# Kernel optimization log

Measured on AMD Instinct MI355X. Metric: run time of the kernel, lower is better.

## Reference

```python
import jax, jax.numpy as jnp
import numpy as np

N_R = 256          # number of relations
N_HOP_MAX = 3      # max hops
N_E = 200_000      # number of entities
N_T = 1_000_000    # number of KB triples
B = 32             # batch size
D_Q = 768          # BERT question embedding dim
D_IN = D_Q + (N_HOP_MAX - 1) * N_R  # input width of dense_inf / dense_att


def setup_inputs() -> dict:
    key = jax.random.key(0)
    ks = jax.random.split(key, 7)
    x = (jax.random.uniform(ks[0], (B, N_E)) < 0.001).astype(jnp.float32)
    h_q = jax.random.normal(ks[1], (B, D_Q), jnp.float32)
    W_inf = jax.random.normal(ks[2], (N_R, D_IN), jnp.float32) * 0.02
    W_att = jax.random.normal(ks[3], (1, D_IN), jnp.float32) * 0.02
    subj_idx = jax.random.randint(ks[4], (N_T,), 0, N_E, jnp.int32)
    rel_idx = jax.random.randint(ks[5], (N_T,), 0, N_R, jnp.int32)
    obj_idx = jax.random.randint(ks[6], (N_T,), 0, N_E, jnp.int32)
    return {"x": x, "h_q": h_q, "W_inf": W_inf, "W_att": W_att,
            "subj_idx": subj_idx, "rel_idx": rel_idx, "obj_idx": obj_idx,
            "n_hop": N_HOP_MAX}


def _one_step(x, r, subj_idx, rel_idx, obj_idx):
    # Equivalent to ((x @ M_subj.T) * (r @ M_rel.T)) @ M_obj with 0/1
    # indicator matrices: gather - elementwise multiply - scatter-add.
    x_t = jnp.take(x, subj_idx, axis=1)   # (B, N_T)
    r_t = jnp.take(r, rel_idx, axis=1)    # (B, N_T)
    prod = x_t * r_t                       # (B, N_T)
    # scatter-add over triples into object entities: (N_T, B) -> (N_E, B)
    return jax.ops.segment_sum(prod.T, obj_idx, num_segments=x.shape[1]).T


def reference(x, h_q, W_inf, W_att, subj_idx, rel_idx, obj_idx, n_hop):
    rs, cs, xs = [], [], []
    for i in range(n_hop):
        if i:
            # most-recent relation first, then older ones (rs[::-1])
            concat = jnp.concatenate([h_q] + rs[::-1], axis=1)
        else:
            concat = h_q
        pad = jnp.zeros((h_q.shape[0], (N_HOP_MAX - 1 - i) * N_R), h_q.dtype)
        concat = jnp.concatenate([concat, pad], axis=1)  # (B, D_IN)
        r = concat @ W_inf.T   # (B, N_R)
        c = concat @ W_att.T   # (B, 1)
        x = _one_step(x, r, subj_idx, rel_idx, obj_idx)  # (B, N_E)
        rs.append(r)
        cs.append(c)
        xs.append(x)
    a = jax.nn.softmax(jnp.concatenate(cs, axis=1), axis=-1)  # (B, n_hop)
    y = jnp.einsum('bh,bhe->be', a, jnp.stack(xs, axis=1))     # (B, N_E)
    return y
```

## Files before the change

kernel.cpp:

```cpp
#include <hip/hip_runtime.h>

#define N_R   256
#define N_E   200000
#define N_T   1000000
#define D_Q   768
#define D_IN  1280
#define NHB   3907

template <bool BN>
__device__ __forceinline__ void hop_one(
        const float* __restrict__ xIn, const unsigned* __restrict__ maskIn,
        const float* __restrict__ rT,
        const int* __restrict__ subj, const int* __restrict__ rel,
        const int* __restrict__ obj,
        float* __restrict__ xOut, unsigned* __restrict__ maskOut, int tid) {
    if (tid >= N_T) return;
    int s = subj[tid];
    int r = rel[tid];
    int o = obj[tid];
    unsigned mm = maskIn[s];
    if (!mm) return;
    atomicOr(&maskOut[o], mm);
    const float* rrow = rT + r * 32;
    while (mm) {
        int bb = __ffs(mm) - 1;
        mm &= mm - 1;
        float v = BN ? xIn[(size_t)bb * N_E + s] : xIn[(size_t)s * 32 + bb];
        unsafeAtomicAdd(&xOut[(size_t)o * 32 + bb], v * rrow[bb]);
    }
}

__global__ void kA(const float* __restrict__ x, const float* __restrict__ h_q,
                   const float* __restrict__ W_inf,
                   unsigned* __restrict__ mask0, unsigned* __restrict__ mask1,
                   unsigned* __restrict__ mask2, float* __restrict__ rT0) {
    __shared__ float hs[32 * 257];
    __shared__ float red[256];
    int t = threadIdx.x;
    if (blockIdx.x < 782) {
        int tid = blockIdx.x * 256 + t;
        if (tid < N_E) {
            unsigned m = 0;
#pragma unroll 8
            for (int b = 0; b < 32; ++b)
                m |= (x[(size_t)b * N_E + tid] != 0.f ? 1u : 0u) << b;
            mask0[tid] = m;
            mask1[tid] = 0u;
            mask2[tid] = 0u;
        }
    } else {
        int rel = blockIdx.x - 782;
        int b = t & 31, kp = t >> 5;
        float acc = 0.f;
        for (int c = 0; c < 3; ++c) {
            __syncthreads();
#pragma unroll
            for (int i = 0; i < 32; ++i)
                hs[i * 257 + t] = h_q[i * D_Q + c * 256 + t];
            __syncthreads();
            const float* w = &W_inf[rel * D_IN + c * 256 + kp * 32];
#pragma unroll
            for (int i = 0; i < 32; ++i)
                acc += w[i] * hs[b * 257 + kp * 32 + i];
        }
        red[t] = acc;
        __syncthreads();
        if (t < 32) {
            float s = 0.f;
            for (int q = 0; q < 8; ++q) s += red[q * 32 + t];
            rT0[rel * 32 + t] = s;
        }
    }
}

__global__ void kB(const float* __restrict__ W_inf, const float* __restrict__ rT0,
                   float* __restrict__ rT1,
                   const float* __restrict__ x, const unsigned* __restrict__ mask0,
                   const int* __restrict__ subj, const int* __restrict__ rel,
                   const int* __restrict__ obj,
                   float* __restrict__ bufA, unsigned* __restrict__ mask1) {
    __shared__ float red[256];
    int t = threadIdx.x;
    if (blockIdx.x < 256) {
        int relb = blockIdx.x;
        int b = t & 31, jp = t >> 5;
        const float* w2 = &W_inf[relb * D_IN + D_Q];
        float acc = 0.f;
#pragma unroll 8
        for (int jj = 0; jj < 32; ++jj) {
            int j = jp * 32 + jj;
            acc += w2[j] * rT0[j * 32 + b];
        }
        red[t] = acc;
        __syncthreads();
        if (t < 32) {
            float s = rT0[relb * 32 + t];
            for (int q = 0; q < 8; ++q) s += red[q * 32 + t];
            rT1[relb * 32 + t] = s;
        }
    } else {
        hop_one<true>(x, mask0, rT0, subj, rel, obj, bufA, mask1,
                      (blockIdx.x - 256) * 256 + t);
    }
}

__global__ void kC(const float* __restrict__ W_inf, const float* __restrict__ W_att,
                   const float* __restrict__ h_q,
                   const float* __restrict__ rT0, const float* __restrict__ rT1,
                   float* __restrict__ rT2, float* __restrict__ a_w,
                   const float* __restrict__ bufA, const unsigned* __restrict__ mask1,
                   const int* __restrict__ subj, const int* __restrict__ rel,
                   const int* __restrict__ obj,
                   float* __restrict__ bufB, unsigned* __restrict__ mask2,
                   float4* __restrict__ outv) {
    __shared__ float red[256];
    __shared__ float p0[256], p1[256], p2[256], p3[256];
    int t = threadIdx.x;
    if (blockIdx.x < 256) {
        int relb = blockIdx.x;
        int b = t & 31, jp = t >> 5;
        const float* w2 = &W_inf[relb * D_IN + D_Q];
        const float* w3 = w2 + N_R;
        float acc = 0.f;
#pragma unroll 8
        for (int jj = 0; jj < 32; ++jj) {
            int j = jp * 32 + jj;
            acc += w2[j] * rT1[j * 32 + b] + w3[j] * rT0[j * 32 + b];
        }
        red[t] = acc;
        __syncthreads();
        if (t < 32) {
            float s = rT0[relb * 32 + t];
            for (int q = 0; q < 8; ++q) s += red[q * 32 + t];
            rT2[relb * 32 + t] = s;
        }
    } else if (blockIdx.x == 256) {
        int b = t & 31, p = t >> 5;
        float c0 = 0.f;
        for (int k = p * 96; k < p * 96 + 96; ++k) c0 += W_att[k] * h_q[b * D_Q + k];
        float s1 = 0.f, s2 = 0.f, s3 = 0.f;
        for (int j = p * 32; j < p * 32 + 32; ++j) {
            float w2 = W_att[D_Q + j], w3 = W_att[D_Q + N_R + j];
            float r0v = rT0[j * 32 + b], r1v = rT1[j * 32 + b];
            s1 += w2 * r0v; s2 += w2 * r1v; s3 += w3 * r0v;
        }
        p0[t] = c0; p1[t] = s1; p2[t] = s2; p3[t] = s3;
        __syncthreads();
        if (t < 32) {
            float C0 = 0.f, S1 = 0.f, S2 = 0.f, S3 = 0.f;
            for (int q = 0; q < 8; ++q) {
                C0 += p0[q * 32 + t]; S1 += p1[q * 32 + t];
                S2 += p2[q * 32 + t]; S3 += p3[q * 32 + t];
            }
            float c1 = C0 + S1, c2 = C0 + S2 + S3;
            float m  = fmaxf(C0, fmaxf(c1, c2));
            float e0 = __expf(C0 - m), e1 = __expf(c1 - m), e2 = __expf(c2 - m);
            float inv = 1.f / (e0 + e1 + e2);
            a_w[t] = e0 * inv; a_w[32 + t] = e1 * inv; a_w[64 + t] = e2 * inv;
        }
    } else {
        int hb  = blockIdx.x - 257;
        int tid = hb * 256 + t;
        float4 z = {0.f, 0.f, 0.f, 0.f};
        for (int i = tid; i < 1600000; i += NHB * 256) outv[i] = z;
        hop_one<false>(bufA, mask1, rT1, subj, rel, obj, bufB, mask2, tid);
    }
}

__global__ void kDE(const float* __restrict__ bufA, const float* __restrict__ bufB,
                    const unsigned* __restrict__ mask1,
                    const unsigned* __restrict__ mask2,
                    const float* __restrict__ rT2, const float* __restrict__ a_w,
                    const int* __restrict__ subj, const int* __restrict__ rel,
                    const int* __restrict__ obj, float* __restrict__ out) {
    __shared__ float a0s[32], a1s[32], a2s[32];
    int t = threadIdx.x;
    if (t < 32) { a0s[t] = a_w[t]; a1s[t] = a_w[32 + t]; a2s[t] = a_w[64 + t]; }
    __syncthreads();
    if (blockIdx.x < NHB) {
        int tid = blockIdx.x * 256 + t;
        if (tid >= N_T) return;
        int s = subj[tid];
        int r = rel[tid];
        int o = obj[tid];
        unsigned mm = mask2[s];
        if (!mm) return;
        const float* rrow = rT2 + r * 32;
        const float* xrow = bufB + (size_t)s * 32;
        while (mm) {
            int bb = __ffs(mm) - 1;
            mm &= mm - 1;
            unsafeAtomicAdd(&out[(size_t)bb * N_E + o],
                            a2s[bb] * xrow[bb] * rrow[bb]);
        }
    } else {
        int e = (blockIdx.x - NHB) * 256 + t;
        if (e >= N_E) return;
        unsigned m1v = mask1[e], m2v = mask2[e];
        unsigned mu = m1v | m2v;
        if (!mu) return;
        const float* r1 = bufA + (size_t)e * 32;
        const float* r2 = bufB + (size_t)e * 32;
        while (mu) {
            int bb = __ffs(mu) - 1;
            mu &= mu - 1;
            float c = 0.f;
            if ((m1v >> bb) & 1) c += a0s[bb] * r1[bb];
            if ((m2v >> bb) & 1) c += a1s[bb] * r2[bb];
            unsafeAtomicAdd(&out[(size_t)bb * N_E + e], c);
        }
    }
}

extern "C" void kernel_launch(void* const* d_in, const int* in_sizes, int n_in,
                              void* d_out, int out_size, void* d_ws, size_t ws_size,
                              hipStream_t stream) {
    const float* x     = (const float*)d_in[0];
    const float* h_q   = (const float*)d_in[1];
    const float* W_inf = (const float*)d_in[2];
    const float* W_att = (const float*)d_in[3];
    const int*   subj  = (const int*)d_in[4];
    const int*   rel   = (const int*)d_in[5];
    const int*   obj   = (const int*)d_in[6];
    float* out = (float*)d_out;

    const size_t NEB = (size_t)N_E * 32;
    float*    bufA  = (float*)d_ws;
    float*    bufB  = bufA + NEB;
    float*    rT0   = bufB + NEB;
    float*    rT1   = rT0 + N_R * 32;
    float*    rT2   = rT1 + N_R * 32;
    float*    a_w   = rT2 + N_R * 32;
    unsigned* mask0 = (unsigned*)(a_w + 96);
    unsigned* mask1 = mask0 + N_E;
    unsigned* mask2 = mask1 + N_E;

    kA<<<782 + 256, 256, 0, stream>>>(x, h_q, W_inf, mask0, mask1, mask2, rT0);
    kB<<<256 + NHB, 256, 0, stream>>>(W_inf, rT0, rT1, x, mask0,
                                      subj, rel, obj, bufA, mask1);
    kC<<<257 + NHB, 256, 0, stream>>>(W_inf, W_att, h_q, rT0, rT1, rT2, a_w,
                                      bufA, mask1, subj, rel, obj,
                                      bufB, mask2, (float4*)out);
    kDE<<<NHB + 782, 256, 0, stream>>>(bufA, bufB, mask1, mask2, rT2, a_w,
                                       subj, rel, obj, out);
}
```

Baseline: 187.1 us.

## Split hop kernels from dense relation kernels and use nontemporal triple loads

```diff
diff --git a/kernel.cpp b/kernel.cpp
--- a/kernel.cpp
+++ b/kernel.cpp
@@ -6,6 +6,8 @@
 #define D_Q   768
 #define D_IN  1280
 #define NHB   3907
+
+typedef float vfloat4 __attribute__((ext_vector_type(4)));
 
 template <bool BN>
 __device__ __forceinline__ void hop_one(
@@ -15,9 +17,9 @@
         const int* __restrict__ obj,
         float* __restrict__ xOut, unsigned* __restrict__ maskOut, int tid) {
     if (tid >= N_T) return;
-    int s = subj[tid];
-    int r = rel[tid];
-    int o = obj[tid];
+    int s = __builtin_nontemporal_load(&subj[tid]);
+    int r = __builtin_nontemporal_load(&rel[tid]);
+    int o = __builtin_nontemporal_load(&obj[tid]);
     unsigned mm = maskIn[s];
     if (!mm) return;
     atomicOr(&maskOut[o], mm);
@@ -73,46 +75,32 @@
     }
 }
 
-__global__ void kB(const float* __restrict__ W_inf, const float* __restrict__ rT0,
-                   float* __restrict__ rT1,
-                   const float* __restrict__ x, const unsigned* __restrict__ mask0,
-                   const int* __restrict__ subj, const int* __restrict__ rel,
-                   const int* __restrict__ obj,
-                   float* __restrict__ bufA, unsigned* __restrict__ mask1) {
+__global__ void kB1(const float* __restrict__ W_inf, const float* __restrict__ rT0,
+                    float* __restrict__ rT1) {
     __shared__ float red[256];
     int t = threadIdx.x;
-    if (blockIdx.x < 256) {
-        int relb = blockIdx.x;
-        int b = t & 31, jp = t >> 5;
-        const float* w2 = &W_inf[relb * D_IN + D_Q];
-        float acc = 0.f;
+    int relb = blockIdx.x;
+    int b = t & 31, jp = t >> 5;
+    const float* w2 = &W_inf[relb * D_IN + D_Q];
+    float acc = 0.f;
 #pragma unroll 8
-        for (int jj = 0; jj < 32; ++jj) {
-            int j = jp * 32 + jj;
-            acc += w2[j] * rT0[j * 32 + b];
-        }
-        red[t] = acc;
-        __syncthreads();
-        if (t < 32) {
-            float s = rT0[relb * 32 + t];
-            for (int q = 0; q < 8; ++q) s += red[q * 32 + t];
-            rT1[relb * 32 + t] = s;
-        }
-    } else {
-        hop_one<true>(x, mask0, rT0, subj, rel, obj, bufA, mask1,
-                      (blockIdx.x - 256) * 256 + t);
-    }
-}
-
-__global__ void kC(const float* __restrict__ W_inf, const float* __restrict__ W_att,
-                   const float* __restrict__ h_q,
-                   const float* __restrict__ rT0, const float* __restrict__ rT1,
-                   float* __restrict__ rT2, float* __restrict__ a_w,
-                   const float* __restrict__ bufA, const unsigned* __restrict__ mask1,
-                   const int* __restrict__ subj, const int* __restrict__ rel,
-                   const int* __restrict__ obj,
-                   float* __restrict__ bufB, unsigned* __restrict__ mask2,
-                   float4* __restrict__ outv) {
+    for (int jj = 0; jj < 32; ++jj) {
+        int j = jp * 32 + jj;
+        acc += w2[j] * rT0[j * 32 + b];
+    }
+    red[t] = acc;
+    __syncthreads();
+    if (t < 32) {
+        float s = rT0[relb * 32 + t];
+        for (int q = 0; q < 8; ++q) s += red[q * 32 + t];
+        rT1[relb * 32 + t] = s;
+    }
+}
+
+__global__ void kC1(const float* __restrict__ W_inf, const float* __restrict__ W_att,
+                    const float* __restrict__ h_q,
+                    const float* __restrict__ rT0, const float* __restrict__ rT1,
+                    float* __restrict__ rT2, float* __restrict__ a_w) {
     __shared__ float red[256];
     __shared__ float p0[256], p1[256], p2[256], p3[256];
     int t = threadIdx.x;
@@ -134,7 +122,7 @@
             for (int q = 0; q < 8; ++q) s += red[q * 32 + t];
             rT2[relb * 32 + t] = s;
         }
-    } else if (blockIdx.x == 256) {
+    } else {
         int b = t & 31, p = t >> 5;
         float c0 = 0.f;
         for (int k = p * 96; k < p * 96 + 96; ++k) c0 += W_att[k] * h_q[b * D_Q + k];
@@ -158,13 +146,29 @@
             float inv = 1.f / (e0 + e1 + e2);
             a_w[t] = e0 * inv; a_w[32 + t] = e1 * inv; a_w[64 + t] = e2 * inv;
         }
-    } else {
-        int hb  = blockIdx.x - 257;
-        int tid = hb * 256 + t;
-        float4 z = {0.f, 0.f, 0.f, 0.f};
-        for (int i = tid; i < 1600000; i += NHB * 256) outv[i] = z;
-        hop_one<false>(bufA, mask1, rT1, subj, rel, obj, bufB, mask2, tid);
-    }
+    }
+}
+
+__global__ void kB2(const float* __restrict__ x, const unsigned* __restrict__ mask0,
+                    const float* __restrict__ rT0,
+                    const int* __restrict__ subj, const int* __restrict__ rel,
+                    const int* __restrict__ obj,
+                    float* __restrict__ bufA, unsigned* __restrict__ mask1,
+                    vfloat4* __restrict__ outv) {
+    int tid = blockIdx.x * 256 + threadIdx.x;
+    vfloat4 z = {0.f, 0.f, 0.f, 0.f};
+    for (int i = tid; i < 1600000; i += NHB * 256)
+        __builtin_nontemporal_store(z, &outv[i]);
+    hop_one<true>(x, mask0, rT0, subj, rel, obj, bufA, mask1, tid);
+}
+
+__global__ void kC2(const float* __restrict__ bufA, const unsigned* __restrict__ mask1,
+                    const float* __restrict__ rT1,
+                    const int* __restrict__ subj, const int* __restrict__ rel,
+                    const int* __restrict__ obj,
+                    float* __restrict__ bufB, unsigned* __restrict__ mask2) {
+    hop_one<false>(bufA, mask1, rT1, subj, rel, obj, bufB, mask2,
+                   blockIdx.x * 256 + threadIdx.x);
 }
 
 __global__ void kDE(const float* __restrict__ bufA, const float* __restrict__ bufB,
@@ -180,9 +184,9 @@
     if (blockIdx.x < NHB) {
         int tid = blockIdx.x * 256 + t;
         if (tid >= N_T) return;
-        int s = subj[tid];
-        int r = rel[tid];
-        int o = obj[tid];
+        int s = __builtin_nontemporal_load(&subj[tid]);
+        int r = __builtin_nontemporal_load(&rel[tid]);
+        int o = __builtin_nontemporal_load(&obj[tid]);
         unsigned mm = mask2[s];
         if (!mm) return;
         const float* rrow = rT2 + r * 32;
@@ -194,20 +198,25 @@
                             a2s[bb] * xrow[bb] * rrow[bb]);
         }
     } else {
-        int e = (blockIdx.x - NHB) * 256 + t;
-        if (e >= N_E) return;
-        unsigned m1v = mask1[e], m2v = mask2[e];
-        unsigned mu = m1v | m2v;
-        if (!mu) return;
-        const float* r1 = bufA + (size_t)e * 32;
-        const float* r2 = bufB + (size_t)e * 32;
-        while (mu) {
-            int bb = __ffs(mu) - 1;
-            mu &= mu - 1;
+        int gb  = blockIdx.x - NHB;
+        int sub = t >> 5;
+        int b   = t & 31;
+        for (int e8 = gb; e8 < 25000; e8 += 782) {
+            int e = e8 * 8 + sub;
+            unsigned m1v = mask1[e], m2v = mask2[e];
+            unsigned mu = m1v | m2v;
+            if (!mu) continue;
             float c = 0.f;
-            if ((m1v >> bb) & 1) c += a0s[bb] * r1[bb];
-            if ((m2v >> bb) & 1) c += a1s[bb] * r2[bb];
-            unsafeAtomicAdd(&out[(size_t)bb * N_E + e], c);
+            if (m1v) {
+                float v = bufA[(size_t)e * 32 + b];
+                if ((m1v >> b) & 1) c += a0s[b] * v;
+            }
+            if (m2v) {
+                float v = bufB[(size_t)e * 32 + b];
+                if ((m2v >> b) & 1) c += a1s[b] * v;
+            }
+            if ((mu >> b) & 1)
+                unsafeAtomicAdd(&out[(size_t)b * N_E + e], c);
         }
     }
 }
@@ -236,11 +245,11 @@
     unsigned* mask2 = mask1 + N_E;
 
     kA<<<782 + 256, 256, 0, stream>>>(x, h_q, W_inf, mask0, mask1, mask2, rT0);
-    kB<<<256 + NHB, 256, 0, stream>>>(W_inf, rT0, rT1, x, mask0,
-                                      subj, rel, obj, bufA, mask1);
-    kC<<<257 + NHB, 256, 0, stream>>>(W_inf, W_att, h_q, rT0, rT1, rT2, a_w,
-                                      bufA, mask1, subj, rel, obj,
-                                      bufB, mask2, (float4*)out);
+    kB1<<<256, 256, 0, stream>>>(W_inf, rT0, rT1);
+    kC1<<<257, 256, 0, stream>>>(W_inf, W_att, h_q, rT0, rT1, rT2, a_w);
+    kB2<<<NHB, 256, 0, stream>>>(x, mask0, rT0, subj, rel, obj, bufA, mask1,
+                                 (vfloat4*)out);
+    kC2<<<NHB, 256, 0, stream>>>(bufA, mask1, rT1, subj, rel, obj, bufB, mask2);
     kDE<<<NHB + 782, 256, 0, stream>>>(bufA, bufB, mask1, mask2, rT2, a_w,
                                        subj, rel, obj, out);
 }
```

Result: slower. 223.1 us (+19.2%).
